# Kernel optimization log

Measured on AMD Instinct MI355X. Metric: run time of the kernel, lower is better.

Reference implementation:

```python
import jax, jax.numpy as jnp
import numpy as np

D = 256   # feature_dim
NQ = 512  # num query keypoints
NK = 512  # num key/value keypoints


def setup_inputs() -> dict:
    key = jax.random.key(0)
    ks = jax.random.split(key, 10)
    def w(k, shape, fan_in):
        return jax.random.normal(k, shape, dtype=jnp.float32) / np.sqrt(fan_in)
    inp = {
        "x": jax.random.normal(ks[0], (1, D, NQ), dtype=jnp.float32),
        "source": jax.random.normal(ks[1], (1, D, NK), dtype=jnp.float32),
        # MLPAttention score MLP: Conv1d(2D->D,k=1), ReLU, Conv1d(D->1,k=1)
        "w1": w(ks[2], (D, 2 * D), 2 * D),
        "b1": w(ks[3], (D,), 2 * D),
        "w2": w(ks[4], (1, D), D),
        "b2": w(ks[5], (1,), D),
        # outer MLP: Conv1d(2D->2D,k=1), ReLU, Conv1d(2D->D,k=1) with zero bias init
        "wa": w(ks[6], (2 * D, 2 * D), 2 * D),
        "ba": w(ks[7], (2 * D,), 2 * D),
        "wb": w(ks[8], (D, 2 * D), 2 * D),
        "bb": jnp.zeros((D,), dtype=jnp.float32),
    }
    return inp


def reference(x, source, w1, b1, w2, b2, wa, ba, wb, bb):
    d = x.shape[1]
    q = x[0]       # [D, nq]
    k = source[0]  # [D, nk]
    # cat((q broadcast over nk, k broadcast over nq)) then Conv1d(2D->D) is
    # equivalent to splitting w1 into query/key halves and broadcasting:
    w1q, w1k = w1[:, :d], w1[:, d:]
    aq = w1q @ q + b1[:, None]                       # [D, nq]
    ak = w1k @ k                                     # [D, nk]
    h = jax.nn.relu(aq[:, :, None] + ak[:, None, :])  # [D, nq, nk]
    scores = (jnp.einsum('d,dnm->nm', w2[0], h) + b2[0])[None]  # [1, nq, nk]
    prob = jax.nn.softmax(scores, axis=-1)
    message = jnp.einsum('bnm,bdm->bdn', prob, source)  # [1, D, nq]
    # outer MLP on cat([x, message], channel dim)
    cat = jnp.concatenate([x, message], axis=1)         # [1, 2D, nq]
    h2 = jax.nn.relu(jnp.einsum('oc,bcn->bon', wa, cat) + ba[None, :, None])
    y = jnp.einsum('oc,bcn->bon', wb, h2) + bb[None, :, None]  # [1, D, nq]
    return (y, scores)
```

## Files before the change

kernel.cpp:

```cpp
#include <hip/hip_runtime.h>
#include <hip/hip_bf16.h>

#define DD 256
#define NN 512

typedef __attribute__((ext_vector_type(8))) short short8;
typedef __attribute__((ext_vector_type(4))) float floatx4;

__device__ __forceinline__ unsigned short f2bf(float f) {
  unsigned u = __float_as_uint(f);
  u += 0x7FFFu + ((u >> 16) & 1u);
  return (unsigned short)(u >> 16);
}
__device__ __forceinline__ unsigned pack2(float a, float b) {
  return (unsigned)f2bf(a) | ((unsigned)f2bf(b) << 16);
}

__device__ __forceinline__ short8 ldfrag(const unsigned short* __restrict__ base,
                                         int row, int ld, int k, int lane) {
  return *(const short8*)(base + (row + (lane & 15)) * ld + k + ((lane >> 4) << 3));
}

template <int NF>
__device__ __forceinline__ void acc_zero(floatx4 acc[NF]) {
#pragma unroll
  for (int i = 0; i < NF; ++i) {
    acc[i][0] = 0.f; acc[i][1] = 0.f; acc[i][2] = 0.f; acc[i][3] = 0.f;
  }
}

template <int NF>
__device__ __forceinline__ void gemm_acc(floatx4 acc[NF],
    const unsigned short* __restrict__ A, int lda, int a_k0,
    const unsigned short* __restrict__ BT, int ldb, int b_k0,
    int K, int m0, int n0, int lane) {
  for (int k = 0; k < K; k += 32) {
    short8 a = ldfrag(A, m0, lda, a_k0 + k, lane);
#pragma unroll
    for (int nf = 0; nf < NF; ++nf) {
      short8 b = ldfrag(BT, n0 + nf * 16, ldb, b_k0 + k, lane);
      acc[nf] = __builtin_amdgcn_mfma_f32_16x16x32_bf16(a, b, acc[nf], 0, 0, 0);
    }
  }
}

template <int NF>
__device__ __forceinline__ void ksplit_combine(floatx4 acc[NF], float* red,
                                               int wave, int lane) {
  const int W = 16 * NF;
  const int col = lane & 15;
  const int q = lane >> 4;
  if (wave > 0) {
    float* base = red + (wave - 1) * 16 * W;
#pragma unroll
    for (int nf = 0; nf < NF; ++nf)
#pragma unroll
      for (int r = 0; r < 4; ++r)
        base[(q * 4 + r) * W + nf * 16 + col] = acc[nf][r];
  }
  __syncthreads();
  if (wave == 0) {
#pragma unroll
    for (int nf = 0; nf < NF; ++nf)
#pragma unroll
      for (int r = 0; r < 4; ++r) {
        const int idx = (q * 4 + r) * W + nf * 16 + col;
        acc[nf][r] += red[idx] + red[16 * W + idx] + red[32 * W + idx];
      }
  }
}

template <int NF, bool COLBIAS, bool ROWBIAS, bool RELU, bool OUTBF>
__device__ __forceinline__ void gemm_epi(floatx4 acc[NF],
    const float* __restrict__ bias, void* __restrict__ C, int ldc,
    int m0, int n0, int lane) {
  const int col = lane & 15;
  const int q = lane >> 4;
#pragma unroll
  for (int nf = 0; nf < NF; ++nf) {
    const int n = n0 + nf * 16 + col;
    const float cb = COLBIAS ? bias[n] : 0.0f;
#pragma unroll
    for (int r = 0; r < 4; ++r) {
      const int m = m0 + q * 4 + r;
      float v = acc[nf][r] + cb + (ROWBIAS ? bias[m] : 0.0f);
      if (RELU) v = fmaxf(v, 0.0f);
      if (OUTBF) ((unsigned short*)C)[m * ldc + n] = f2bf(v);
      else       ((float*)C)[m * ldc + n] = v;
    }
  }
}

__global__ __launch_bounds__(256) void prep_kernel(
    const float* __restrict__ x, const float* __restrict__ src,
    const float* __restrict__ w1, const float* __restrict__ wa,
    const float* __restrict__ wb, const float* __restrict__ b2,
    unsigned short* __restrict__ w1b, unsigned short* __restrict__ wab,
    unsigned short* __restrict__ wbb, unsigned short* __restrict__ srcb,
    unsigned short* __restrict__ xT, unsigned short* __restrict__ srcT,
    float* __restrict__ sc) {
  const int bid = blockIdx.x;
  const int tid = threadIdx.x;
  if (bid < 640) {
    const float* in; unsigned short* out; int off;
    if (bid < 128)      { in = w1;  out = w1b; off = bid; }
    else if (bid < 384) { in = wa;  out = wab; off = bid - 128; }
    else if (bid < 512) { in = wb;  out = wbb; off = bid - 384; }
    else                { in = src; out = srcb; off = bid - 512; }
    const int i = off * 1024 + tid * 4;
    const float4 v = *(const float4*)(in + i);
    *(uint2*)(out + i) = make_uint2(pack2(v.x, v.y), pack2(v.z, v.w));
  } else if (bid < 896) {
    __shared__ float tile[32][33];
    const int b = bid - 640;
    const float* in = (b >> 7) ? src : x;
    unsigned short* out = (b >> 7) ? srcT : xT;
    const int t = b & 127;
    const int n0 = (t >> 3) * 32;
    const int d0 = (t & 7) * 32;
    const int tx = tid & 31, ty = tid >> 5;
#pragma unroll
    for (int i = ty; i < 32; i += 8)
      tile[i][tx] = in[(d0 + i) * NN + n0 + tx];
    __syncthreads();
#pragma unroll
    for (int i = ty; i < 32; i += 8)
      out[(n0 + i) * DD + d0 + tx] = f2bf(tile[tx][i]);
  } else {
    const float bv = b2[0];
    const int i = (bid - 896) * 1024 + tid * 4;
    float4 o; o.x = bv; o.y = bv; o.z = bv; o.w = bv;
    *(float4*)(sc + i) = o;
  }
}

__global__ __launch_bounds__(256) void aqak_kernel(
    const unsigned short* __restrict__ xT, const unsigned short* __restrict__ srcT,
    const unsigned short* __restrict__ w1b, const float* __restrict__ b1,
    float* __restrict__ aq, float* __restrict__ ak) {
  __shared__ float red[1536];
  const int tid = threadIdx.x;
  const int lane = tid & 63;
  const int wave = tid >> 6;
  const int m0 = blockIdx.y * 16;
  const int n0 = blockIdx.x * 32;
  const int z = blockIdx.z;
  const unsigned short* BT = z ? srcT : xT;

  floatx4 acc[2]; acc_zero<2>(acc);
  gemm_acc<2>(acc, w1b, NN, z * 256 + wave * 64, BT, DD, wave * 64, 64, m0, n0, lane);
  ksplit_combine<2>(acc, red, wave, lane);
  if (wave == 0) {
    if (z == 0) gemm_epi<2, false, true, false, false>(acc, b1, aq, NN, m0, n0, lane);
    else        gemm_epi<2, false, false, false, false>(acc, nullptr, ak, NN, m0, n0, lane);
  }
}

__global__ __launch_bounds__(256) void scores_kernel(
    const float* __restrict__ aq, const float* __restrict__ ak,
    const float* __restrict__ w2, float* __restrict__ sc) {
  __shared__ float aqs[128][32];
  __shared__ float aks[128][32];
  __shared__ float w2s[128];

  const int tid = threadIdx.x;
  const int n0 = blockIdx.x * 32;
  const int m0 = blockIdx.y * 32;
  const int d0 = blockIdx.z * 128;
  const int tn = tid & 31;
  const int tm4 = (tid >> 5) * 4;

  if (tid < 128) w2s[tid] = w2[d0 + tid];
#pragma unroll
  for (int k = 0; k < 16; ++k) {
    const int idx = k * 256 + tid;
    const int r = idx >> 5, cc = idx & 31;
    aqs[r][cc] = aq[(d0 + r) * NN + n0 + cc];
    aks[r][cc] = ak[(d0 + r) * NN + m0 + cc];
  }
  __syncthreads();

  float s0 = 0.f, s1 = 0.f, s2 = 0.f, s3 = 0.f;
  for (int dd = 0; dd < 128; ++dd) {
    const float w = w2s[dd];
    const float a = aqs[dd][tn];
    const float4 akv = *(const float4*)&aks[dd][tm4];
    s0 += w * fmaxf(a + akv.x, 0.f);
    s1 += w * fmaxf(a + akv.y, 0.f);
    s2 += w * fmaxf(a + akv.z, 0.f);
    s3 += w * fmaxf(a + akv.w, 0.f);
  }

  float* p = &sc[(n0 + tn) * NN + m0 + tm4];
  atomicAdd(p + 0, s0);
  atomicAdd(p + 1, s1);
  atomicAdd(p + 2, s2);
  atomicAdd(p + 3, s3);
}

__global__ __launch_bounds__(256) void msgT_kernel(
    const float* __restrict__ sc, const unsigned short* __restrict__ srcb,
    unsigned short* __restrict__ msgTb) {
  __shared__ unsigned short Ap[16][520];
  __shared__ float red[1536];
  __shared__ float smax[16][16];
  __shared__ float ssum[16][16];
  __shared__ float rst[16][2];

  const int tid = threadIdx.x;
  const int lane = tid & 63;
  const int wave = tid >> 6;
  const int n0 = blockIdx.y * 16;
  const int d0 = blockIdx.x * 32;

  const int r = tid >> 4;
  const int c = tid & 15;
  float4 v[8];
  const float* rp = sc + (n0 + r) * NN + c * 4;
#pragma unroll
  for (int i = 0; i < 8; ++i) v[i] = *(const float4*)(rp + i * 64);

  float mx = -3.0e38f;
#pragma unroll
  for (int i = 0; i < 8; ++i)
    mx = fmaxf(mx, fmaxf(fmaxf(v[i].x, v[i].y), fmaxf(v[i].z, v[i].w)));
  smax[r][c] = mx;
  __syncthreads();
  if (c == 0) {
    float m2 = smax[r][0];
#pragma unroll
    for (int i = 1; i < 16; ++i) m2 = fmaxf(m2, smax[r][i]);
    rst[r][0] = m2;
  }
  __syncthreads();
  mx = rst[r][0];

  float sum = 0.f;
#pragma unroll
  for (int i = 0; i < 8; ++i) {
    v[i].x = __expf(v[i].x - mx); v[i].y = __expf(v[i].y - mx);
    v[i].z = __expf(v[i].z - mx); v[i].w = __expf(v[i].w - mx);
    sum += v[i].x + v[i].y + v[i].z + v[i].w;
  }
  ssum[r][c] = sum;
  __syncthreads();
  if (c == 0) {
    float s2 = ssum[r][0];
#pragma unroll
    for (int i = 1; i < 16; ++i) s2 += ssum[r][i];
    rst[r][1] = s2;
  }
  __syncthreads();
  const float inv = 1.0f / rst[r][1];
#pragma unroll
  for (int i = 0; i < 8; ++i) {
    *(unsigned*)&Ap[r][c * 4 + i * 64]     = pack2(v[i].x * inv, v[i].y * inv);
    *(unsigned*)&Ap[r][c * 4 + i * 64 + 2] = pack2(v[i].z * inv, v[i].w * inv);
  }
  __syncthreads();

  floatx4 acc[2]; acc_zero<2>(acc);
  const int k0w = wave * 128;
  const int arow = lane & 15;
  const int koff = (lane >> 4) << 3;
  for (int k = 0; k < 128; k += 32) {
    short8 a = *(const short8*)&Ap[arow][k0w + k + koff];
#pragma unroll
    for (int nf = 0; nf < 2; ++nf) {
      short8 b = ldfrag(srcb, d0 + nf * 16, NN, k0w + k, lane);
      acc[nf] = __builtin_amdgcn_mfma_f32_16x16x32_bf16(a, b, acc[nf], 0, 0, 0);
    }
  }
  ksplit_combine<2>(acc, red, wave, lane);
  if (wave == 0)
    gemm_epi<2, false, false, false, true>(acc, nullptr, msgTb, DD, n0, d0, lane);
}

__global__ __launch_bounds__(256) void h2T_kernel(
    const unsigned short* __restrict__ xT, const unsigned short* __restrict__ msgTb,
    const unsigned short* __restrict__ wab, const float* __restrict__ ba,
    unsigned short* __restrict__ h2Tb) {
  __shared__ float red[1536];
  const int tid = threadIdx.x;
  const int lane = tid & 63;
  const int wave = tid >> 6;
  const int m0 = blockIdx.y * 16;
  const int n0 = blockIdx.x * 32;

  floatx4 acc[2]; acc_zero<2>(acc);
  const unsigned short* A = (wave < 2) ? xT : msgTb;
  gemm_acc<2>(acc, A, DD, (wave & 1) * 128, wab, NN, wave * 128, 128, m0, n0, lane);
  ksplit_combine<2>(acc, red, wave, lane);
  if (wave == 0)
    gemm_epi<2, true, false, true, true>(acc, ba, h2Tb, NN, m0, n0, lane);
}

__global__ __launch_bounds__(256) void y_kernel(
    const unsigned short* __restrict__ wbb, const unsigned short* __restrict__ h2Tb,
    const float* __restrict__ bb, float* __restrict__ y) {
  __shared__ float red[1536];
  const int tid = threadIdx.x;
  const int lane = tid & 63;
  const int wave = tid >> 6;
  const int m0 = blockIdx.y * 16;
  const int n0 = blockIdx.x * 32;

  floatx4 acc[2]; acc_zero<2>(acc);
  gemm_acc<2>(acc, wbb, NN, wave * 128, h2Tb, NN, wave * 128, 128, m0, n0, lane);
  ksplit_combine<2>(acc, red, wave, lane);
  if (wave == 0)
    gemm_epi<2, false, true, false, false>(acc, bb, y, NN, m0, n0, lane);
}

extern "C" void kernel_launch(void* const* d_in, const int* in_sizes, int n_in,
                              void* d_out, int out_size, void* d_ws, size_t ws_size,
                              hipStream_t stream) {
  (void)in_sizes; (void)n_in; (void)out_size; (void)ws_size;

  const float* x   = (const float*)d_in[0];
  const float* src = (const float*)d_in[1];
  const float* w1  = (const float*)d_in[2];
  const float* b1  = (const float*)d_in[3];
  const float* w2  = (const float*)d_in[4];
  const float* b2  = (const float*)d_in[5];
  const float* wa  = (const float*)d_in[6];
  const float* ba  = (const float*)d_in[7];
  const float* wb  = (const float*)d_in[8];
  const float* bb  = (const float*)d_in[9];

  float* y_out  = (float*)d_out;
  float* sc_out = (float*)d_out + 131072;

  char* ws = (char*)d_ws;
  unsigned short* w1b   = (unsigned short*)(ws);
  unsigned short* wab   = (unsigned short*)(ws + (256 << 10));
  unsigned short* wbb   = (unsigned short*)(ws + (768 << 10));
  unsigned short* srcb  = (unsigned short*)(ws + (1024 << 10));
  unsigned short* xT    = (unsigned short*)(ws + (1280 << 10));
  unsigned short* srcT  = (unsigned short*)(ws + (1536 << 10));
  unsigned short* msgTb = (unsigned short*)(ws + (1792 << 10));
  unsigned short* h2Tb  = (unsigned short*)(ws + (2048 << 10));
  float*          aq    = (float*)(ws + (2560 << 10));
  float*          ak    = (float*)(ws + (3072 << 10));

  prep_kernel<<<1152, 256, 0, stream>>>(x, src, w1, wa, wb, b2,
                                        w1b, wab, wbb, srcb, xT, srcT, sc_out);
  aqak_kernel<<<dim3(16, 16, 2), 256, 0, stream>>>(xT, srcT, w1b, b1, aq, ak);
  scores_kernel<<<dim3(16, 16, 2), 256, 0, stream>>>(aq, ak, w2, sc_out);
  msgT_kernel<<<dim3(8, 32), 256, 0, stream>>>(sc_out, srcb, msgTb);
  h2T_kernel<<<dim3(16, 32), 256, 0, stream>>>(xT, msgTb, wab, ba, h2Tb);
  y_kernel<<<dim3(16, 16), 256, 0, stream>>>(wbb, h2Tb, bb, y_out);
}
```

Before: 112.7 us.

## Fuse five stage kernels into one persistent kernel with grid barriers

Replaces the aq/ak, scores, softmax-message, h2 and y kernels with one 256-block persistent kernel that separates the stages with a software grid barrier. This is meant to remove per-launch overhead and the tail gaps between stages. The scores stage now loops over the full feature dimension in one block and writes the scores directly with the bias added, so the bias-fill pass and the atomic adds go away. Each stage has fewer blocks, and the spin barrier relies on all 256 blocks being co-resident on the device.

```diff
diff --git a/kernel.cpp b/kernel.cpp
--- a/kernel.cpp
+++ b/kernel.cpp
@@ -29,11 +29,12 @@
   }
 }
 
-template <int NF>
+template <int NF, int K>
 __device__ __forceinline__ void gemm_acc(floatx4 acc[NF],
     const unsigned short* __restrict__ A, int lda, int a_k0,
     const unsigned short* __restrict__ BT, int ldb, int b_k0,
-    int K, int m0, int n0, int lane) {
+    int m0, int n0, int lane) {
+#pragma unroll
   for (int k = 0; k < K; k += 32) {
     short8 a = ldfrag(A, m0, lda, a_k0 + k, lane);
 #pragma unroll
@@ -91,16 +92,37 @@
   }
 }
 
+__device__ __forceinline__ void gridbar(unsigned* cnt, unsigned* gen, unsigned nb) {
+  __syncthreads();
+  if (threadIdx.x == 0) {
+    __threadfence();
+    const unsigned g = __hip_atomic_load(gen, __ATOMIC_RELAXED, __HIP_MEMORY_SCOPE_AGENT);
+    const unsigned a = __hip_atomic_fetch_add(cnt, 1u, __ATOMIC_RELAXED, __HIP_MEMORY_SCOPE_AGENT);
+    if (a == nb - 1u) {
+      __threadfence();
+      __hip_atomic_store(cnt, 0u, __ATOMIC_RELAXED, __HIP_MEMORY_SCOPE_AGENT);
+      __threadfence();
+      __hip_atomic_fetch_add(gen, 1u, __ATOMIC_RELAXED, __HIP_MEMORY_SCOPE_AGENT);
+    } else {
+      while (__hip_atomic_load(gen, __ATOMIC_RELAXED, __HIP_MEMORY_SCOPE_AGENT) == g)
+        __builtin_amdgcn_s_sleep(2);
+      __threadfence();
+    }
+  }
+  __syncthreads();
+}
+
 __global__ __launch_bounds__(256) void prep_kernel(
     const float* __restrict__ x, const float* __restrict__ src,
     const float* __restrict__ w1, const float* __restrict__ wa,
-    const float* __restrict__ wb, const float* __restrict__ b2,
+    const float* __restrict__ wb,
     unsigned short* __restrict__ w1b, unsigned short* __restrict__ wab,
     unsigned short* __restrict__ wbb, unsigned short* __restrict__ srcb,
     unsigned short* __restrict__ xT, unsigned short* __restrict__ srcT,
-    float* __restrict__ sc) {
+    unsigned* __restrict__ bar) {
   const int bid = blockIdx.x;
   const int tid = threadIdx.x;
+  if (bid == 0 && tid < 8) bar[tid] = 0u;
   if (bid < 640) {
     const float* in; unsigned short* out; int off;
     if (bid < 128)      { in = w1;  out = w1b; off = bid; }
@@ -110,7 +132,7 @@
     const int i = off * 1024 + tid * 4;
     const float4 v = *(const float4*)(in + i);
     *(uint2*)(out + i) = make_uint2(pack2(v.x, v.y), pack2(v.z, v.w));
-  } else if (bid < 896) {
+  } else {
     __shared__ float tile[32][33];
     const int b = bid - 640;
     const float* in = (b >> 7) ? src : x;
@@ -126,190 +148,198 @@
 #pragma unroll
     for (int i = ty; i < 32; i += 8)
       out[(n0 + i) * DD + d0 + tx] = f2bf(tile[tx][i]);
-  } else {
-    const float bv = b2[0];
-    const int i = (bid - 896) * 1024 + tid * 4;
-    float4 o; o.x = bv; o.y = bv; o.z = bv; o.w = bv;
-    *(float4*)(sc + i) = o;
-  }
-}
-
-__global__ __launch_bounds__(256) void aqak_kernel(
-    const unsigned short* __restrict__ xT, const unsigned short* __restrict__ srcT,
-    const unsigned short* __restrict__ w1b, const float* __restrict__ b1,
-    float* __restrict__ aq, float* __restrict__ ak) {
-  __shared__ float red[1536];
+  }
+}
+
+__global__ __launch_bounds__(256) void mega_kernel(
+    const unsigned short* __restrict__ w1b, const unsigned short* __restrict__ xT,
+    const unsigned short* __restrict__ srcT, const unsigned short* __restrict__ srcb,
+    const unsigned short* __restrict__ wab, const unsigned short* __restrict__ wbb,
+    const float* __restrict__ b1, const float* __restrict__ w2,
+    const float* __restrict__ b2, const float* __restrict__ ba,
+    const float* __restrict__ bb,
+    float* __restrict__ aq, float* __restrict__ ak,
+    unsigned short* __restrict__ msgTb, unsigned short* __restrict__ h2Tb,
+    float* __restrict__ sc, float* __restrict__ y,
+    unsigned* __restrict__ bar) {
+  __shared__ __align__(16) char smem[33792];
+  const int bid = blockIdx.x;
   const int tid = threadIdx.x;
   const int lane = tid & 63;
   const int wave = tid >> 6;
-  const int m0 = blockIdx.y * 16;
-  const int n0 = blockIdx.x * 32;
-  const int z = blockIdx.z;
-  const unsigned short* BT = z ? srcT : xT;
-
-  floatx4 acc[2]; acc_zero<2>(acc);
-  gemm_acc<2>(acc, w1b, NN, z * 256 + wave * 64, BT, DD, wave * 64, 64, m0, n0, lane);
-  ksplit_combine<2>(acc, red, wave, lane);
-  if (wave == 0) {
-    if (z == 0) gemm_epi<2, false, true, false, false>(acc, b1, aq, NN, m0, n0, lane);
-    else        gemm_epi<2, false, false, false, false>(acc, nullptr, ak, NN, m0, n0, lane);
-  }
-}
-
-__global__ __launch_bounds__(256) void scores_kernel(
-    const float* __restrict__ aq, const float* __restrict__ ak,
-    const float* __restrict__ w2, float* __restrict__ sc) {
-  __shared__ float aqs[128][32];
-  __shared__ float aks[128][32];
-  __shared__ float w2s[128];
-
-  const int tid = threadIdx.x;
-  const int n0 = blockIdx.x * 32;
-  const int m0 = blockIdx.y * 32;
-  const int d0 = blockIdx.z * 128;
-  const int tn = tid & 31;
-  const int tm4 = (tid >> 5) * 4;
-
-  if (tid < 128) w2s[tid] = w2[d0 + tid];
-#pragma unroll
-  for (int k = 0; k < 16; ++k) {
-    const int idx = k * 256 + tid;
-    const int r = idx >> 5, cc = idx & 31;
-    aqs[r][cc] = aq[(d0 + r) * NN + n0 + cc];
-    aks[r][cc] = ak[(d0 + r) * NN + m0 + cc];
-  }
-  __syncthreads();
-
-  float s0 = 0.f, s1 = 0.f, s2 = 0.f, s3 = 0.f;
-  for (int dd = 0; dd < 128; ++dd) {
-    const float w = w2s[dd];
-    const float a = aqs[dd][tn];
-    const float4 akv = *(const float4*)&aks[dd][tm4];
-    s0 += w * fmaxf(a + akv.x, 0.f);
-    s1 += w * fmaxf(a + akv.y, 0.f);
-    s2 += w * fmaxf(a + akv.z, 0.f);
-    s3 += w * fmaxf(a + akv.w, 0.f);
-  }
-
-  float* p = &sc[(n0 + tn) * NN + m0 + tm4];
-  atomicAdd(p + 0, s0);
-  atomicAdd(p + 1, s1);
-  atomicAdd(p + 2, s2);
-  atomicAdd(p + 3, s3);
-}
-
-__global__ __launch_bounds__(256) void msgT_kernel(
-    const float* __restrict__ sc, const unsigned short* __restrict__ srcb,
-    unsigned short* __restrict__ msgTb) {
-  __shared__ unsigned short Ap[16][520];
-  __shared__ float red[1536];
-  __shared__ float smax[16][16];
-  __shared__ float ssum[16][16];
-  __shared__ float rst[16][2];
-
-  const int tid = threadIdx.x;
-  const int lane = tid & 63;
-  const int wave = tid >> 6;
-  const int n0 = blockIdx.y * 16;
-  const int d0 = blockIdx.x * 32;
-
-  const int r = tid >> 4;
-  const int c = tid & 15;
-  float4 v[8];
-  const float* rp = sc + (n0 + r) * NN + c * 4;
-#pragma unroll
-  for (int i = 0; i < 8; ++i) v[i] = *(const float4*)(rp + i * 64);
-
-  float mx = -3.0e38f;
-#pragma unroll
-  for (int i = 0; i < 8; ++i)
-    mx = fmaxf(mx, fmaxf(fmaxf(v[i].x, v[i].y), fmaxf(v[i].z, v[i].w)));
-  smax[r][c] = mx;
-  __syncthreads();
-  if (c == 0) {
-    float m2 = smax[r][0];
-#pragma unroll
-    for (int i = 1; i < 16; ++i) m2 = fmaxf(m2, smax[r][i]);
-    rst[r][0] = m2;
-  }
-  __syncthreads();
-  mx = rst[r][0];
-
-  float sum = 0.f;
-#pragma unroll
-  for (int i = 0; i < 8; ++i) {
-    v[i].x = __expf(v[i].x - mx); v[i].y = __expf(v[i].y - mx);
-    v[i].z = __expf(v[i].z - mx); v[i].w = __expf(v[i].w - mx);
-    sum += v[i].x + v[i].y + v[i].z + v[i].w;
-  }
-  ssum[r][c] = sum;
-  __syncthreads();
-  if (c == 0) {
-    float s2 = ssum[r][0];
-#pragma unroll
-    for (int i = 1; i < 16; ++i) s2 += ssum[r][i];
-    rst[r][1] = s2;
-  }
-  __syncthreads();
-  const float inv = 1.0f / rst[r][1];
-#pragma unroll
-  for (int i = 0; i < 8; ++i) {
-    *(unsigned*)&Ap[r][c * 4 + i * 64]     = pack2(v[i].x * inv, v[i].y * inv);
-    *(unsigned*)&Ap[r][c * 4 + i * 64 + 2] = pack2(v[i].z * inv, v[i].w * inv);
-  }
-  __syncthreads();
-
-  floatx4 acc[2]; acc_zero<2>(acc);
-  const int k0w = wave * 128;
-  const int arow = lane & 15;
-  const int koff = (lane >> 4) << 3;
-  for (int k = 0; k < 128; k += 32) {
-    short8 a = *(const short8*)&Ap[arow][k0w + k + koff];
-#pragma unroll
-    for (int nf = 0; nf < 2; ++nf) {
-      short8 b = ldfrag(srcb, d0 + nf * 16, NN, k0w + k, lane);
-      acc[nf] = __builtin_amdgcn_mfma_f32_16x16x32_bf16(a, b, acc[nf], 0, 0, 0);
-    }
-  }
-  ksplit_combine<2>(acc, red, wave, lane);
-  if (wave == 0)
-    gemm_epi<2, false, false, false, true>(acc, nullptr, msgTb, DD, n0, d0, lane);
-}
-
-__global__ __launch_bounds__(256) void h2T_kernel(
-    const unsigned short* __restrict__ xT, const unsigned short* __restrict__ msgTb,
-    const unsigned short* __restrict__ wab, const float* __restrict__ ba,
-    unsigned short* __restrict__ h2Tb) {
-  __shared__ float red[1536];
-  const int tid = threadIdx.x;
-  const int lane = tid & 63;
-  const int wave = tid >> 6;
-  const int m0 = blockIdx.y * 16;
-  const int n0 = blockIdx.x * 32;
-
-  floatx4 acc[2]; acc_zero<2>(acc);
-  const unsigned short* A = (wave < 2) ? xT : msgTb;
-  gemm_acc<2>(acc, A, DD, (wave & 1) * 128, wab, NN, wave * 128, 128, m0, n0, lane);
-  ksplit_combine<2>(acc, red, wave, lane);
-  if (wave == 0)
-    gemm_epi<2, true, false, true, true>(acc, ba, h2Tb, NN, m0, n0, lane);
-}
-
-__global__ __launch_bounds__(256) void y_kernel(
-    const unsigned short* __restrict__ wbb, const unsigned short* __restrict__ h2Tb,
-    const float* __restrict__ bb, float* __restrict__ y) {
-  __shared__ float red[1536];
-  const int tid = threadIdx.x;
-  const int lane = tid & 63;
-  const int wave = tid >> 6;
-  const int m0 = blockIdx.y * 16;
-  const int n0 = blockIdx.x * 32;
-
-  floatx4 acc[2]; acc_zero<2>(acc);
-  gemm_acc<2>(acc, wbb, NN, wave * 128, h2Tb, NN, wave * 128, 128, m0, n0, lane);
-  ksplit_combine<2>(acc, red, wave, lane);
-  if (wave == 0)
-    gemm_epi<2, false, true, false, false>(acc, bb, y, NN, m0, n0, lane);
+  unsigned* cnt = bar;
+  unsigned* gen = bar + 4;
+
+  {
+    float* red = (float*)smem;
+    const int job = bid * 4 + wave;
+    const int z = job >> 9;
+    const int ks = job & 1;
+    const int tile = (job >> 1) & 255;
+    const int m0 = (tile >> 4) * 16;
+    const int n0 = (tile & 15) * 32;
+    const unsigned short* BT = z ? srcT : xT;
+
+    floatx4 acc[2]; acc_zero<2>(acc);
+    gemm_acc<2, 128>(acc, w1b, NN, z * 256 + ks * 128, BT, DD, ks * 128, m0, n0, lane);
+
+    const int col = lane & 15, q = lane >> 4;
+    float* base = red + (wave >> 1) * 512;
+    if (wave & 1) {
+#pragma unroll
+      for (int nf = 0; nf < 2; ++nf)
+#pragma unroll
+        for (int r = 0; r < 4; ++r)
+          base[(q * 4 + r) * 32 + nf * 16 + col] = acc[nf][r];
+    }
+    __syncthreads();
+    if (!(wave & 1)) {
+#pragma unroll
+      for (int nf = 0; nf < 2; ++nf)
+#pragma unroll
+        for (int r = 0; r < 4; ++r)
+          acc[nf][r] += base[(q * 4 + r) * 32 + nf * 16 + col];
+      if (z == 0) gemm_epi<2, false, true, false, false>(acc, b1, aq, NN, m0, n0, lane);
+      else        gemm_epi<2, false, false, false, false>(acc, nullptr, ak, NN, m0, n0, lane);
+    }
+  }
+  gridbar(cnt, gen, 256);
+
+  {
+    float (*aqs)[32] = (float(*)[32])smem;
+    float (*aks)[32] = (float(*)[32])(smem + 16384);
+    float* w2s = (float*)(smem + 32768);
+    const int n0 = (bid >> 4) * 32;
+    const int m0 = (bid & 15) * 32;
+    const int tn = tid & 31;
+    const int tm4 = (tid >> 5) * 4;
+
+    w2s[tid] = w2[tid];
+
+    float s0 = 0.f, s1 = 0.f, s2 = 0.f, s3 = 0.f;
+    for (int d0 = 0; d0 < DD; d0 += 128) {
+      __syncthreads();
+#pragma unroll
+      for (int k = 0; k < 16; ++k) {
+        const int idx = k * 256 + tid;
+        const int r = idx >> 5, cc = idx & 31;
+        aqs[r][cc] = aq[(d0 + r) * NN + n0 + cc];
+        aks[r][cc] = ak[(d0 + r) * NN + m0 + cc];
+      }
+      __syncthreads();
+      for (int dd = 0; dd < 128; ++dd) {
+        const float w = w2s[d0 + dd];
+        const float a = aqs[dd][tn];
+        const float4 akv = *(const float4*)&aks[dd][tm4];
+        s0 += w * fmaxf(a + akv.x, 0.f);
+        s1 += w * fmaxf(a + akv.y, 0.f);
+        s2 += w * fmaxf(a + akv.z, 0.f);
+        s3 += w * fmaxf(a + akv.w, 0.f);
+      }
+    }
+    const float bv = b2[0];
+    float4 o; o.x = s0 + bv; o.y = s1 + bv; o.z = s2 + bv; o.w = s3 + bv;
+    *(float4*)&sc[(n0 + tn) * NN + m0 + tm4] = o;
+  }
+  gridbar(cnt, gen, 256);
+
+  {
+    unsigned short (*Ap)[520] = (unsigned short(*)[520])smem;
+    float* red  = (float*)(smem + 16640);
+    float (*smax)[16] = (float(*)[16])(smem + 22784);
+    float (*ssum)[16] = (float(*)[16])(smem + 23808);
+    float (*rst)[2]   = (float(*)[2])(smem + 24832);
+    const int n0 = (bid >> 3) * 16;
+    const int d0 = (bid & 7) * 32;
+
+    const int r = tid >> 4;
+    const int c = tid & 15;
+    float4 v[8];
+    const float* rp = sc + (n0 + r) * NN + c * 4;
+#pragma unroll
+    for (int i = 0; i < 8; ++i) v[i] = *(const float4*)(rp + i * 64);
+
+    float mx = -3.0e38f;
+#pragma unroll
+    for (int i = 0; i < 8; ++i)
+      mx = fmaxf(mx, fmaxf(fmaxf(v[i].x, v[i].y), fmaxf(v[i].z, v[i].w)));
+    smax[r][c] = mx;
+    __syncthreads();
+    if (c == 0) {
+      float m2 = smax[r][0];
+#pragma unroll
+      for (int i = 1; i < 16; ++i) m2 = fmaxf(m2, smax[r][i]);
+      rst[r][0] = m2;
+    }
+    __syncthreads();
+    mx = rst[r][0];
+
+    float sum = 0.f;
+#pragma unroll
+    for (int i = 0; i < 8; ++i) {
+      v[i].x = __expf(v[i].x - mx); v[i].y = __expf(v[i].y - mx);
+      v[i].z = __expf(v[i].z - mx); v[i].w = __expf(v[i].w - mx);
+      sum += v[i].x + v[i].y + v[i].z + v[i].w;
+    }
+    ssum[r][c] = sum;
+    __syncthreads();
+    if (c == 0) {
+      float s2 = ssum[r][0];
+#pragma unroll
+      for (int i = 1; i < 16; ++i) s2 += ssum[r][i];
+      rst[r][1] = s2;
+    }
+    __syncthreads();
+    const float inv = 1.0f / rst[r][1];
+#pragma unroll
+    for (int i = 0; i < 8; ++i) {
+      *(unsigned*)&Ap[r][c * 4 + i * 64]     = pack2(v[i].x * inv, v[i].y * inv);
+      *(unsigned*)&Ap[r][c * 4 + i * 64 + 2] = pack2(v[i].z * inv, v[i].w * inv);
+    }
+    __syncthreads();
+
+    floatx4 acc[2]; acc_zero<2>(acc);
+    const int k0w = wave * 128;
+    const int arow = lane & 15;
+    const int koff = (lane >> 4) << 3;
+#pragma unroll
+    for (int k = 0; k < 128; k += 32) {
+      short8 a = *(const short8*)&Ap[arow][k0w + k + koff];
+#pragma unroll
+      for (int nf = 0; nf < 2; ++nf) {
+        short8 b = ldfrag(srcb, d0 + nf * 16, NN, k0w + k, lane);
+        acc[nf] = __builtin_amdgcn_mfma_f32_16x16x32_bf16(a, b, acc[nf], 0, 0, 0);
+      }
+    }
+    ksplit_combine<2>(acc, red, wave, lane);
+    if (wave == 0)
+      gemm_epi<2, false, false, false, true>(acc, nullptr, msgTb, DD, n0, d0, lane);
+  }
+  gridbar(cnt, gen, 256);
+
+  {
+    float* red = (float*)smem;
+    const int m0 = (bid >> 3) * 16;
+    const int n0 = (bid & 7) * 64;
+    floatx4 acc[4]; acc_zero<4>(acc);
+    const unsigned short* A = (wave < 2) ? xT : msgTb;
+    gemm_acc<4, 128>(acc, A, DD, (wave & 1) * 128, wab, NN, wave * 128, m0, n0, lane);
+    ksplit_combine<4>(acc, red, wave, lane);
+    if (wave == 0)
+      gemm_epi<4, true, false, true, true>(acc, ba, h2Tb, NN, m0, n0, lane);
+  }
+  gridbar(cnt, gen, 256);
+
+  {
+    float* red = (float*)smem;
+    const int m0 = (bid >> 4) * 16;
+    const int n0 = (bid & 15) * 32;
+    floatx4 acc[2]; acc_zero<2>(acc);
+    gemm_acc<2, 128>(acc, wbb, NN, wave * 128, h2Tb, NN, wave * 128, m0, n0, lane);
+    ksplit_combine<2>(acc, red, wave, lane);
+    if (wave == 0)
+      gemm_epi<2, false, true, false, false>(acc, bb, y, NN, m0, n0, lane);
+  }
 }
 
 extern "C" void kernel_launch(void* const* d_in, const int* in_sizes, int n_in,
@@ -342,12 +372,11 @@
   unsigned short* h2Tb  = (unsigned short*)(ws + (2048 << 10));
   float*          aq    = (float*)(ws + (2560 << 10));
   float*          ak    = (float*)(ws + (3072 << 10));
-
-  prep_kernel<<<1152, 256, 0, stream>>>(x, src, w1, wa, wb, b2,
-                                        w1b, wab, wbb, srcb, xT, srcT, sc_out);
-  aqak_kernel<<<dim3(16, 16, 2), 256, 0, stream>>>(xT, srcT, w1b, b1, aq, ak);
-  scores_kernel<<<dim3(16, 16, 2), 256, 0, stream>>>(aq, ak, w2, sc_out);
-  msgT_kernel<<<dim3(8, 32), 256, 0, stream>>>(sc_out, srcb, msgTb);
-  h2T_kernel<<<dim3(16, 32), 256, 0, stream>>>(xT, msgTb, wab, ba, h2Tb);
-  y_kernel<<<dim3(16, 16), 256, 0, stream>>>(wbb, h2Tb, bb, y_out);
-}
+  unsigned*       bar   = (unsigned*)(ws + (3584 << 10));
+
+  prep_kernel<<<896, 256, 0, stream>>>(x, src, w1, wa, wb,
+                                       w1b, wab, wbb, srcb, xT, srcT, bar);
+  mega_kernel<<<256, 256, 0, stream>>>(w1b, xT, srcT, srcb, wab, wbb,
+                                       b1, w2, b2, ba, bb,
+                                       aq, ak, msgTb, h2Tb, sc_out, y_out, bar);
+}
```

Measured after the change: 208.9 us. 1.85x slower.

## Fuse aq/ak projection into scores kernel and fuse outer MLP layers

Applied to the files above, without the earlier changes.

Merges the aq/ak GEMM with the score computation in one kernel. Each 32x32 score tile recomputes its aq/ak slices with MFMA into bf16 shared memory, then reduces over d across waves without atomics. The two outer MLP GEMMs are merged into one kernel that keeps the h2 tile in LDS and atomically accumulates y, which prep now initialises with bb. This cuts the launch count from six to four and removes the intermediate global buffers. The cost is redundant aq/ak recomputation per tile, bf16 rounding of aq/ak in the score path, and atomic adds on y.

```diff
diff --git a/kernel.cpp b/kernel.cpp
--- a/kernel.cpp
+++ b/kernel.cpp
@@ -15,6 +15,8 @@
 __device__ __forceinline__ unsigned pack2(float a, float b) {
   return (unsigned)f2bf(a) | ((unsigned)f2bf(b) << 16);
 }
+__device__ __forceinline__ float bflo(unsigned u) { return __uint_as_float(u << 16); }
+__device__ __forceinline__ float bfhi(unsigned u) { return __uint_as_float(u & 0xFFFF0000u); }
 
 __device__ __forceinline__ short8 ldfrag(const unsigned short* __restrict__ base,
                                          int row, int ld, int k, int lane) {
@@ -26,21 +28,6 @@
 #pragma unroll
   for (int i = 0; i < NF; ++i) {
     acc[i][0] = 0.f; acc[i][1] = 0.f; acc[i][2] = 0.f; acc[i][3] = 0.f;
-  }
-}
-
-template <int NF>
-__device__ __forceinline__ void gemm_acc(floatx4 acc[NF],
-    const unsigned short* __restrict__ A, int lda, int a_k0,
-    const unsigned short* __restrict__ BT, int ldb, int b_k0,
-    int K, int m0, int n0, int lane) {
-  for (int k = 0; k < K; k += 32) {
-    short8 a = ldfrag(A, m0, lda, a_k0 + k, lane);
-#pragma unroll
-    for (int nf = 0; nf < NF; ++nf) {
-      short8 b = ldfrag(BT, n0 + nf * 16, ldb, b_k0 + k, lane);
-      acc[nf] = __builtin_amdgcn_mfma_f32_16x16x32_bf16(a, b, acc[nf], 0, 0, 0);
-    }
   }
 }
 
@@ -94,11 +81,11 @@
 __global__ __launch_bounds__(256) void prep_kernel(
     const float* __restrict__ x, const float* __restrict__ src,
     const float* __restrict__ w1, const float* __restrict__ wa,
-    const float* __restrict__ wb, const float* __restrict__ b2,
+    const float* __restrict__ wb, const float* __restrict__ bb,
     unsigned short* __restrict__ w1b, unsigned short* __restrict__ wab,
     unsigned short* __restrict__ wbb, unsigned short* __restrict__ srcb,
     unsigned short* __restrict__ xT, unsigned short* __restrict__ srcT,
-    float* __restrict__ sc) {
+    float* __restrict__ y) {
   const int bid = blockIdx.x;
   const int tid = threadIdx.x;
   if (bid < 640) {
@@ -127,75 +114,108 @@
     for (int i = ty; i < 32; i += 8)
       out[(n0 + i) * DD + d0 + tx] = f2bf(tile[tx][i]);
   } else {
-    const float bv = b2[0];
     const int i = (bid - 896) * 1024 + tid * 4;
+    const float bv = bb[i >> 9];
     float4 o; o.x = bv; o.y = bv; o.z = bv; o.w = bv;
-    *(float4*)(sc + i) = o;
-  }
-}
-
-__global__ __launch_bounds__(256) void aqak_kernel(
-    const unsigned short* __restrict__ xT, const unsigned short* __restrict__ srcT,
-    const unsigned short* __restrict__ w1b, const float* __restrict__ b1,
-    float* __restrict__ aq, float* __restrict__ ak) {
-  __shared__ float red[1536];
+    *(float4*)(y + i) = o;
+  }
+}
+
+__global__ __launch_bounds__(256) void qks_kernel(
+    const unsigned short* __restrict__ w1b, const unsigned short* __restrict__ xT,
+    const unsigned short* __restrict__ srcT, const float* __restrict__ b1,
+    const float* __restrict__ w2, const float* __restrict__ b2,
+    float* __restrict__ sc) {
+  __shared__ __align__(16) unsigned short aqs[256][36];
+  __shared__ __align__(16) unsigned short aks[256][36];
+  __shared__ __align__(16) float part[4][32][32];
+  __shared__ float w2s[DD];
+
   const int tid = threadIdx.x;
   const int lane = tid & 63;
   const int wave = tid >> 6;
-  const int m0 = blockIdx.y * 16;
-  const int n0 = blockIdx.x * 32;
-  const int z = blockIdx.z;
-  const unsigned short* BT = z ? srcT : xT;
-
-  floatx4 acc[2]; acc_zero<2>(acc);
-  gemm_acc<2>(acc, w1b, NN, z * 256 + wave * 64, BT, DD, wave * 64, 64, m0, n0, lane);
-  ksplit_combine<2>(acc, red, wave, lane);
-  if (wave == 0) {
-    if (z == 0) gemm_epi<2, false, true, false, false>(acc, b1, aq, NN, m0, n0, lane);
-    else        gemm_epi<2, false, false, false, false>(acc, nullptr, ak, NN, m0, n0, lane);
-  }
-}
-
-__global__ __launch_bounds__(256) void scores_kernel(
-    const float* __restrict__ aq, const float* __restrict__ ak,
-    const float* __restrict__ w2, float* __restrict__ sc) {
-  __shared__ float aqs[128][32];
-  __shared__ float aks[128][32];
-  __shared__ float w2s[128];
-
-  const int tid = threadIdx.x;
   const int n0 = blockIdx.x * 32;
   const int m0 = blockIdx.y * 32;
-  const int d0 = blockIdx.z * 128;
-  const int tn = tid & 31;
-  const int tm4 = (tid >> 5) * 4;
-
-  if (tid < 128) w2s[tid] = w2[d0 + tid];
-#pragma unroll
-  for (int k = 0; k < 16; ++k) {
-    const int idx = k * 256 + tid;
-    const int r = idx >> 5, cc = idx & 31;
-    aqs[r][cc] = aq[(d0 + r) * NN + n0 + cc];
-    aks[r][cc] = ak[(d0 + r) * NN + m0 + cc];
-  }
-  __syncthreads();
-
-  float s0 = 0.f, s1 = 0.f, s2 = 0.f, s3 = 0.f;
-  for (int dd = 0; dd < 128; ++dd) {
-    const float w = w2s[dd];
-    const float a = aqs[dd][tn];
-    const float4 akv = *(const float4*)&aks[dd][tm4];
-    s0 += w * fmaxf(a + akv.x, 0.f);
-    s1 += w * fmaxf(a + akv.y, 0.f);
-    s2 += w * fmaxf(a + akv.z, 0.f);
-    s3 += w * fmaxf(a + akv.w, 0.f);
-  }
-
-  float* p = &sc[(n0 + tn) * NN + m0 + tm4];
-  atomicAdd(p + 0, s0);
-  atomicAdd(p + 1, s1);
-  atomicAdd(p + 2, s2);
-  atomicAdd(p + 3, s3);
+
+  w2s[tid] = w2[tid];
+
+  {
+    const int col = lane & 15, q = lane >> 4;
+#pragma unroll
+    for (int j = 0; j < 8; ++j) {
+      const int jid = wave * 8 + j;
+      const int z = jid >> 4;
+      const int d0t = (jid & 15) * 16;
+      const unsigned short* BT = z ? srcT : xT;
+      const int tok0 = z ? m0 : n0;
+      floatx4 acc[2]; acc_zero<2>(acc);
+#pragma unroll
+      for (int kc = 0; kc < 8; ++kc) {
+        const int c0 = kc * 32;
+        short8 a = ldfrag(w1b, d0t, NN, z * 256 + c0, lane);
+#pragma unroll
+        for (int nf = 0; nf < 2; ++nf) {
+          short8 b = ldfrag(BT, tok0 + nf * 16, DD, c0, lane);
+          acc[nf] = __builtin_amdgcn_mfma_f32_16x16x32_bf16(a, b, acc[nf], 0, 0, 0);
+        }
+      }
+#pragma unroll
+      for (int nf = 0; nf < 2; ++nf)
+#pragma unroll
+        for (int r = 0; r < 4; ++r) {
+          const int d = d0t + q * 4 + r;
+          float v = acc[nf][r] + (z ? 0.0f : b1[d]);
+          (z ? aks : aqs)[d][nf * 16 + col] = f2bf(v);
+        }
+    }
+  }
+  __syncthreads();
+
+  {
+    const int nq = lane & 7;
+    const int mq = lane >> 3;
+    float s[4][4];
+#pragma unroll
+    for (int i = 0; i < 4; ++i)
+#pragma unroll
+      for (int j = 0; j < 4; ++j) s[i][j] = 0.f;
+
+    const int dbeg = wave * 64;
+    for (int dd = dbeg; dd < dbeg + 64; ++dd) {
+      const uint2 aw = *(const uint2*)&aqs[dd][nq * 4];
+      const uint2 kw = *(const uint2*)&aks[dd][mq * 4];
+      const float w = w2s[dd];
+      float a[4] = {bflo(aw.x), bfhi(aw.x), bflo(aw.y), bfhi(aw.y)};
+      float k[4] = {bflo(kw.x), bfhi(kw.x), bflo(kw.y), bfhi(kw.y)};
+#pragma unroll
+      for (int i = 0; i < 4; ++i)
+#pragma unroll
+        for (int j = 0; j < 4; ++j)
+          s[i][j] += w * fmaxf(a[i] + k[j], 0.f);
+    }
+#pragma unroll
+    for (int i = 0; i < 4; ++i)
+#pragma unroll
+      for (int j = 0; j < 4; ++j)
+        part[wave][nq * 4 + i][mq * 4 + j] = s[i][j];
+  }
+  __syncthreads();
+
+  {
+    const int n = tid >> 3;
+    const int mg = (tid & 7) * 4;
+    float4 p0 = *(const float4*)&part[0][n][mg];
+    float4 p1 = *(const float4*)&part[1][n][mg];
+    float4 p2 = *(const float4*)&part[2][n][mg];
+    float4 p3 = *(const float4*)&part[3][n][mg];
+    const float bv = b2[0];
+    float4 o;
+    o.x = p0.x + p1.x + p2.x + p3.x + bv;
+    o.y = p0.y + p1.y + p2.y + p3.y + bv;
+    o.z = p0.z + p1.z + p2.z + p3.z + bv;
+    o.w = p0.w + p1.w + p2.w + p3.w + bv;
+    *(float4*)&sc[(n0 + n) * NN + m0 + mg] = o;
+  }
 }
 
 __global__ __launch_bounds__(256) void msgT_kernel(
@@ -263,6 +283,7 @@
   const int k0w = wave * 128;
   const int arow = lane & 15;
   const int koff = (lane >> 4) << 3;
+#pragma unroll
   for (int k = 0; k < 128; k += 32) {
     short8 a = *(const short8*)&Ap[arow][k0w + k + koff];
 #pragma unroll
@@ -276,40 +297,66 @@
     gemm_epi<2, false, false, false, true>(acc, nullptr, msgTb, DD, n0, d0, lane);
 }
 
-__global__ __launch_bounds__(256) void h2T_kernel(
+__global__ __launch_bounds__(256) void h2y_kernel(
     const unsigned short* __restrict__ xT, const unsigned short* __restrict__ msgTb,
-    const unsigned short* __restrict__ wab, const float* __restrict__ ba,
-    unsigned short* __restrict__ h2Tb) {
-  __shared__ float red[1536];
+    const unsigned short* __restrict__ wab, const unsigned short* __restrict__ wbb,
+    const float* __restrict__ ba, float* __restrict__ y) {
+  __shared__ __align__(16) unsigned short h2L[16][144];
+
   const int tid = threadIdx.x;
   const int lane = tid & 63;
   const int wave = tid >> 6;
-  const int m0 = blockIdx.y * 16;
-  const int n0 = blockIdx.x * 32;
-
-  floatx4 acc[2]; acc_zero<2>(acc);
-  const unsigned short* A = (wave < 2) ? xT : msgTb;
-  gemm_acc<2>(acc, A, DD, (wave & 1) * 128, wab, NN, wave * 128, 128, m0, n0, lane);
-  ksplit_combine<2>(acc, red, wave, lane);
-  if (wave == 0)
-    gemm_epi<2, true, false, true, true>(acc, ba, h2Tb, NN, m0, n0, lane);
-}
-
-__global__ __launch_bounds__(256) void y_kernel(
-    const unsigned short* __restrict__ wbb, const unsigned short* __restrict__ h2Tb,
-    const float* __restrict__ bb, float* __restrict__ y) {
-  __shared__ float red[1536];
-  const int tid = threadIdx.x;
-  const int lane = tid & 63;
-  const int wave = tid >> 6;
-  const int m0 = blockIdx.y * 16;
-  const int n0 = blockIdx.x * 32;
-
-  floatx4 acc[2]; acc_zero<2>(acc);
-  gemm_acc<2>(acc, wbb, NN, wave * 128, h2Tb, NN, wave * 128, 128, m0, n0, lane);
-  ksplit_combine<2>(acc, red, wave, lane);
-  if (wave == 0)
-    gemm_epi<2, false, true, false, false>(acc, bb, y, NN, m0, n0, lane);
+  const int nt = blockIdx.x >> 2;
+  const int qh = blockIdx.x & 3;
+  const int n0g = nt * 16;
+  const int o0 = qh * 128;
+
+  {
+    floatx4 acc[2]; acc_zero<2>(acc);
+    const int ow = o0 + wave * 32;
+#pragma unroll
+    for (int kc = 0; kc < 16; ++kc) {
+      const int c0 = kc * 32;
+      short8 a = (c0 < 256) ? ldfrag(xT, n0g, DD, c0, lane)
+                            : ldfrag(msgTb, n0g, DD, c0 - 256, lane);
+#pragma unroll
+      for (int nf = 0; nf < 2; ++nf) {
+        short8 b = ldfrag(wab, ow + nf * 16, NN, c0, lane);
+        acc[nf] = __builtin_amdgcn_mfma_f32_16x16x32_bf16(a, b, acc[nf], 0, 0, 0);
+      }
+    }
+    const int col = lane & 15, q = lane >> 4;
+#pragma unroll
+    for (int nf = 0; nf < 2; ++nf) {
+      const int ol = wave * 32 + nf * 16 + col;
+      const float cb = ba[o0 + ol];
+#pragma unroll
+      for (int r = 0; r < 4; ++r)
+        h2L[q * 4 + r][ol] = f2bf(fmaxf(acc[nf][r] + cb, 0.f));
+    }
+  }
+  __syncthreads();
+
+  {
+    const int brow = lane & 15;
+    const int koff = (lane >> 4) << 3;
+    const int col = lane & 15, q = lane >> 4;
+#pragma unroll
+    for (int t = 0; t < 4; ++t) {
+      const int o2t = wave * 64 + t * 16;
+      floatx4 acc;
+      acc[0] = 0.f; acc[1] = 0.f; acc[2] = 0.f; acc[3] = 0.f;
+#pragma unroll
+      for (int kc = 0; kc < 4; ++kc) {
+        short8 a = ldfrag(wbb, o2t, NN, o0 + kc * 32, lane);
+        short8 b = *(const short8*)&h2L[brow][kc * 32 + koff];
+        acc = __builtin_amdgcn_mfma_f32_16x16x32_bf16(a, b, acc, 0, 0, 0);
+      }
+#pragma unroll
+      for (int r = 0; r < 4; ++r)
+        atomicAdd(&y[(o2t + q * 4 + r) * NN + n0g + col], acc[r]);
+    }
+  }
 }
 
 extern "C" void kernel_launch(void* const* d_in, const int* in_sizes, int n_in,
@@ -339,15 +386,10 @@
   unsigned short* xT    = (unsigned short*)(ws + (1280 << 10));
   unsigned short* srcT  = (unsigned short*)(ws + (1536 << 10));
   unsigned short* msgTb = (unsigned short*)(ws + (1792 << 10));
-  unsigned short* h2Tb  = (unsigned short*)(ws + (2048 << 10));
-  float*          aq    = (float*)(ws + (2560 << 10));
-  float*          ak    = (float*)(ws + (3072 << 10));
-
-  prep_kernel<<<1152, 256, 0, stream>>>(x, src, w1, wa, wb, b2,
-                                        w1b, wab, wbb, srcb, xT, srcT, sc_out);
-  aqak_kernel<<<dim3(16, 16, 2), 256, 0, stream>>>(xT, srcT, w1b, b1, aq, ak);
-  scores_kernel<<<dim3(16, 16, 2), 256, 0, stream>>>(aq, ak, w2, sc_out);
+
+  prep_kernel<<<1024, 256, 0, stream>>>(x, src, w1, wa, wb, bb,
+                                        w1b, wab, wbb, srcb, xT, srcT, y_out);
+  qks_kernel<<<dim3(16, 16), 256, 0, stream>>>(w1b, xT, srcT, b1, w2, b2, sc_out);
   msgT_kernel<<<dim3(8, 32), 256, 0, stream>>>(sc_out, srcb, msgTb);
-  h2T_kernel<<<dim3(16, 32), 256, 0, stream>>>(xT, msgTb, wab, ba, h2Tb);
-  y_kernel<<<dim3(16, 16), 256, 0, stream>>>(wbb, h2Tb, bb, y_out);
-}
+  h2y_kernel<<<128, 256, 0, stream>>>(xT, msgTb, wab, wbb, ba, y_out);
+}
```

Measured after the change: 122.7 us. +8.9%, slower.
